# Optimization experiments

Hardware: AMD Instinct MI355X
Metric: run time of the kernel (lower is better)

## Reference

```python
import jax, jax.numpy as jnp
from jax import lax
import numpy as np

B = 2048; D_IN = 784; H = 256; N_OUT = 10

def setup_inputs() -> dict:
    key = jax.random.key(0)
    ks = jax.random.split(key, 12)
    return {
        "x": jax.random.uniform(ks[0], (B, D_IN), jnp.float32),
        "h1": jax.random.randint(ks[1], (B, H), 0, 2, jnp.int32),
        "h2": jax.random.randint(ks[2], (B, H), 0, 2, jnp.int32),
        "y": jax.random.randint(ks[3], (B, N_OUT), 0, 2, jnp.int32),
        "W1": jax.random.normal(ks[4], (D_IN, H), jnp.float32) * 0.05,
        "b1": jnp.zeros((H,), jnp.float32),
        "W2": jax.random.normal(ks[5], (H, H), jnp.float32) * 0.05,
        "b2": jnp.zeros((H,), jnp.float32),
        "Wout": jax.random.normal(ks[6], (H, N_OUT), jnp.float32) * 0.05,
        "bout": jnp.zeros((N_OUT,), jnp.float32),
        # pre-drawn per-node Bernoulli uniforms, shape [H, B] (scan axis first)
        "u1": jax.random.uniform(ks[7], (H, B), jnp.float32),
        "u2": jax.random.uniform(ks[8], (H, B), jnp.float32),
    }

def _sigmoid_ce(labels, logits):
    # tf.nn.sigmoid_cross_entropy_with_logits, numerically stable
    return jnp.maximum(logits, 0.0) - logits * labels + jnp.log1p(jnp.exp(-jnp.abs(logits)))

def _gibbs_layer(pv, cv, nv, W_in, b_in, W_out, b_out, u):
    """One layer of node-by-node Gibbs resampling.
    pv: [B, P] parents, cv: [B, H] current layer (old values),
    nv: [B, Hn] children, u: [H, B] uniforms. Returns (new cv [B,H], final child logits [B,Hn])."""
    parent_logits = pv @ W_in + b_in          # [B, H]; sigmoid(.) = prob_parents
    next_logits0 = cv @ W_out + b_out         # [B, Hn], recurrently updated

    def step(nl, xs):
        node, w_j, pl_j, u_j = xs             # [B], [Hn], [B], [B]
        nl0 = nl - node[:, None] * w_j[None, :]
        nl1 = nl + (1.0 - node)[:, None] * w_j[None, :]
        lp0 = -jnp.sum(_sigmoid_ce(nv, nl0), axis=-1)
        lp1 = -jnp.sum(_sigmoid_ce(nv, nl1), axis=-1)
        # prob = p1/(p1+p0) with p1 = sigm(pl)*exp(lp1), p0 = (1-sigm(pl))*exp(lp0)
        # == sigmoid(pl + lp1 - lp0)  (same math, stable form)
        prob = jax.nn.sigmoid(pl_j + lp1 - lp0)
        new = (u_j < prob).astype(jnp.float32)
        nl_new = jnp.where(new[:, None] > 0.5, nl1, nl0)
        return nl_new, new

    nl_fin, new_T = lax.scan(step, next_logits0, (cv.T, W_out, parent_logits.T, u))
    return new_T.T, nl_fin

def reference(x, h1, h2, y, W1, b1, W2, b2, Wout, bout, u1, u2):
    h1f = h1.astype(jnp.float32)
    h2f = h2.astype(jnp.float32)
    yf = y.astype(jnp.float32)
    # layer 0: parents=x, children=h2 (old values)
    h1_new, _ = _gibbs_layer(x, h1f, h2f, W1, b1, W2, b2, u1)
    # layer 1: parents=h1_new (already updated), children=y, out layer = output_layer
    h2_new, nl_fin = _gibbs_layer(h1_new, h2f, yf, W2, b2, Wout, bout, u2)
    # pack new states + final output-layer logits into one array [B, H+H+N_OUT]
    return jnp.concatenate([h1_new, h2_new, nl_fin], axis=1)
```

## Files before the change

kernel.cpp:

```cpp
#include <hip/hip_runtime.h>
#include <math.h>

#define NB   2048
#define DIN  784
#define HN   256
#define NOUT 10
#define OSTR (HN + HN + NOUT)

struct Smem {
  float4  sup[4][HN];
  double2 tab[65];
  float   scr[4][16 * 20];
  float   h2o[4][HN];
  float   h1n[4][HN];
  float   tmp[4][HN];
  float   yv [4][16];
};

__device__ __forceinline__ float np_expf(float xf) {
  float q = __fmul_rn(xf, 1.442695040888963f);
  q = __fadd_rn(q, 12582912.0f);
  q = __fsub_rn(q, 12582912.0f);
  float x = __builtin_fmaf(q, -6.93145752e-1f, xf);
  x = __builtin_fmaf(q, -1.42860677e-6f, x);
  float num = __builtin_fmaf(x, 5.082762527590693718096e-04f,
                                6.757896990527504603057e-03f);
  num = __builtin_fmaf(num, x, 5.114512081637298353406e-02f);
  num = __builtin_fmaf(num, x, 2.473615434895520810817e-01f);
  num = __builtin_fmaf(num, x, 7.257664613233124478488e-01f);
  num = __builtin_fmaf(num, x, 9.999999999980870924916e-01f);
  float den = __builtin_fmaf(x, 2.159509375685829852307e-02f,
                                -2.742335390411667452936e-01f);
  den = __builtin_fmaf(den, x, 1.0f);
  float r = __fdiv_rn(num, den);
  int qi = (int)q;
  return __fmul_rn(r, __int_as_float((qi + 127) << 23));
}

__device__ __forceinline__ float np_log1pf(float ef, const double2* __restrict__ tab) {
  if (ef < 0x1p-29f) return ef;
  double t  = 1.0 + (double)ef;
  double kd = rint(t * 64.0);
  int   idx = (int)kd - 64;
  double2 te = tab[idx];
  double c  = kd * 0.015625;
  double s  = (t - c) * te.y;
  double p  = fma(s, -1.0/6.0, 0.2);
  p = fma(p, s, -0.25);
  p = fma(p, s,  1.0/3.0);
  p = fma(p, s, -0.5);
  p = fma(p, s,  1.0);
  p = p * s;
  return (float)(te.x + p);
}

__device__ __forceinline__ float ce32(float l, float label, const double2* __restrict__ tab) {
  float t3 = __fsub_rn(fmaxf(l, 0.0f), __fmul_rn(l, label));
  return __fadd_rn(t3, np_log1pf(np_expf(-fabsf(l)), tab));
}

__device__ __forceinline__ bool decide(float u, float ez) {
  float w = __fadd_rn(1.0f, ez);
  float d = __builtin_fmaf(u, w, -1.0f);
  if (__builtin_expect(fabsf(d) < 1e-5f, 0)) {
    float prob = __fdiv_rn(1.0f, w);
    return u < prob;
  }
  return d < 0.0f;
}

template<int CTRL> __device__ __forceinline__ float dppx(float v) {
  return __int_as_float(__builtin_amdgcn_mov_dpp(__float_as_int(v), CTRL, 0xF, 0xF, true));
}
__device__ __forceinline__ float rdl(float v, int l) {
  return __int_as_float(__builtin_amdgcn_readlane(__float_as_int(v), l));
}

__device__ __forceinline__ float sum10(float c) {
  float c0 = rdl(c, 0), c1 = rdl(c, 1), c2 = rdl(c, 2), c3 = rdl(c, 3);
  float c4 = rdl(c, 4), c5 = rdl(c, 5), c6 = rdl(c, 6), c7 = rdl(c, 7);
  float c8 = rdl(c, 8), c9 = rdl(c, 9);
  float t = __fadd_rn(__fadd_rn(__fadd_rn(c0, c1), __fadd_rn(c2, c3)),
                      __fadd_rn(__fadd_rn(c4, c5), __fadd_rn(c6, c7)));
  t = __fadd_rn(t, c8);
  t = __fadd_rn(t, c9);
  return t;
}

__device__ __forceinline__ float fold256_lds(const float c[4], float* __restrict__ scrw,
                                             int idx, int g) {
  *reinterpret_cast<float4*>(scrw + idx * 20 + 4 * g) = make_float4(c[0], c[1], c[2], c[3]);
  const float4* rp = reinterpret_cast<const float4*>(scrw + idx * 20);
  float4 q0 = rp[0], q1 = rp[1], q2 = rp[2], q3 = rp[3];
  float r = q0.x;
  r = __fadd_rn(r, q0.y); r = __fadd_rn(r, q0.z); r = __fadd_rn(r, q0.w);
  r = __fadd_rn(r, q1.x); r = __fadd_rn(r, q1.y); r = __fadd_rn(r, q1.z); r = __fadd_rn(r, q1.w);
  r = __fadd_rn(r, q2.x); r = __fadd_rn(r, q2.y); r = __fadd_rn(r, q2.z); r = __fadd_rn(r, q2.w);
  r = __fadd_rn(r, q3.x); r = __fadd_rn(r, q3.y); r = __fadd_rn(r, q3.z); r = __fadd_rn(r, q3.w);
  r = __fadd_rn(r, dppx<0xB1>(r));
  r = __fadd_rn(r, dppx<0x4E>(r));
  float B0 = rdl(r, 0), B1 = rdl(r, 4), B2 = rdl(r, 8), B3 = rdl(r, 12);
  return __fadd_rn(__fadd_rn(B0, B1), __fadd_rn(B2, B3));
}

__device__ __forceinline__ float fast_sum256(float loc) {
  float r = loc;
  r = r + dppx<0xB1>(r);
  r = r + dppx<0x4E>(r);
  r = r + dppx<0x124>(r);
  r = r + dppx<0x128>(r);
  return (rdl(r, 0) + rdl(r, 16)) + (rdl(r, 32) + rdl(r, 48));
}

__device__ __forceinline__ float lu_of(float u) {
  if (u < 1e-4f || u > 0.9999f) return __int_as_float(0x7FC00000);
  return __logf(u) - __logf(__fsub_rn(1.0f, u));
}

#define ZBAND 0.05f
#define LN2F  0.6931471805599453f

__global__ __launch_bounds__(256) void stoch_mlp(
    const float* __restrict__ x,  const int* __restrict__ h1,
    const int* __restrict__ h2,   const int* __restrict__ y,
    const float* __restrict__ W1, const float* __restrict__ b1,
    const float* __restrict__ W2, const float* __restrict__ b2,
    const float* __restrict__ Wo, const float* __restrict__ bo,
    const float* __restrict__ u1, const float* __restrict__ u2,
    float* __restrict__ out)
{
  __shared__ Smem sm;
  const int t    = threadIdx.x;
  const int lane = t & 63;
  const int wid  = t >> 6;
  const int b0   = blockIdx.x * 4;
  const int b    = b0 + wid;

  if (t < 65) {
    double c = (double)(t + 64) * 0.015625;
    sm.tab[t] = make_double2(log(c), 64.0 / (double)(t + 64));
  }
  for (int j = lane; j < HN; j += 64) sm.h2o[wid][j] = (float)h2[b * HN + j];
  if (lane < 16) sm.yv[wid][lane] = (lane < NOUT) ? (float)y[b * NOUT + lane] : 0.0f;
  {
    float a0 = 0.0f, a1 = 0.0f, a2 = 0.0f, a3 = 0.0f;
    const float* x0 = x + (size_t)b0 * DIN;
    for (int k = 0; k < DIN; ++k) {
      float wk = W1[k * HN + t];
      a0 = __builtin_fmaf(x0[k],           wk, a0);
      a1 = __builtin_fmaf(x0[DIN   + k],   wk, a1);
      a2 = __builtin_fmaf(x0[2*DIN + k],   wk, a2);
      a3 = __builtin_fmaf(x0[3*DIN + k],   wk, a3);
    }
    float bb = b1[t];
    float4 uv = *reinterpret_cast<const float4*>(u1 + (size_t)t * NB + b0);
    float n0 = (float)h1[(b0 + 0) * HN + t];
    float n1 = (float)h1[(b0 + 1) * HN + t];
    float n2 = (float)h1[(b0 + 2) * HN + t];
    float n3 = (float)h1[(b0 + 3) * HN + t];
    sm.sup[0][t] = make_float4(n0, uv.x, __fadd_rn(a0, bb), lu_of(uv.x));
    sm.sup[1][t] = make_float4(n1, uv.y, __fadd_rn(a1, bb), lu_of(uv.y));
    sm.sup[2][t] = make_float4(n2, uv.z, __fadd_rn(a2, bb), lu_of(uv.z));
    sm.sup[3][t] = make_float4(n3, uv.w, __fadd_rn(a3, bb), lu_of(uv.w));
  }
  __syncthreads();

  const double2* tab = sm.tab;
  float* scrw = &sm.scr[wid][0];

  {
    float acc[4] = {0.0f, 0.0f, 0.0f, 0.0f};
    for (int j = 0; j < HN; ++j) {
      float nodej = sm.sup[wid][j].x;
      float4 wf = *reinterpret_cast<const float4*>(W2 + (size_t)j * HN + 4*lane);
      acc[0] = __builtin_fmaf(nodej, wf.x, acc[0]);
      acc[1] = __builtin_fmaf(nodej, wf.y, acc[1]);
      acc[2] = __builtin_fmaf(nodej, wf.z, acc[2]);
      acc[3] = __builtin_fmaf(nodej, wf.w, acc[3]);
    }
    float4 bv = *reinterpret_cast<const float4*>(b2 + 4*lane);
    *reinterpret_cast<float4*>(&sm.tmp[wid][4*lane]) =
        make_float4(__fadd_rn(acc[0], bv.x), __fadd_rn(acc[1], bv.y),
                    __fadd_rn(acc[2], bv.z), __fadd_rn(acc[3], bv.w));
  }

  const int idx  = lane & 15;
  const int g    = lane >> 4;
  const int half = idx >> 3;
  const int jacc = idx & 7;
  const int kb   = half * 128 + (4 * g) * 8 + jacc;

  float nlv[4], nv[4], wv[4];
  int   smk[4];
  #pragma unroll
  for (int i = 0; i < 4; ++i) {
    int k = kb + i * 8;
    nlv[i] = sm.tmp[wid][k];
    nv[i]  = sm.h2o[wid][k];
    smk[i] = (nv[i] != 0.0f) ? (int)0x80000000 : 0;
    wv[i]  = W2[k];
  }
  float S_c;
  {
    float ci[4];
    #pragma unroll
    for (int i = 0; i < 4; ++i) ci[i] = ce32(nlv[i], nv[i], tab);
    S_c = fold256_lds(ci, scrw, idx, g);
  }

  {
    float4 supC = sm.sup[wid][0];
    for (int j = 0; j < HN; ++j) {
      float node = supC.x, uj = supC.y, plj = supC.z, luj = supC.w;
      bool  nd   = (node != 0.0f);
      int   jn   = (j + 1) & (HN - 1);
      float4 supN = sm.sup[wid][jn];
      float wn[4];
      #pragma unroll
      for (int i = 0; i < 4; ++i) wn[i] = W2[(size_t)jn * HN + kb + i * 8];

      int ndm = nd ? (int)0x80000000 : 0;
      float fresh[4], t3[4], p[4];
      #pragma unroll
      for (int i = 0; i < 4; ++i) {
        float ws = __int_as_float(__float_as_int(wv[i]) ^ ndm);
        fresh[i] = __fadd_rn(nlv[i], ws);
        float sl = __int_as_float(__float_as_int(fresh[i]) ^ smk[i]);
        t3[i] = fmaxf(sl, 0.0f);
        p[i]  = __log2f(__fadd_rn(1.0f, __expf(-fabsf(fresh[i]))));
      }
      float T = (t3[0] + t3[1]) + (t3[2] + t3[3]);
      float P = (p[0]  + p[1])  + (p[2]  + p[3]);
      float F = fast_sum256(__builtin_fmaf(LN2F, P, T));
      float sgn = nd ? 1.0f : -1.0f;
      float z = __builtin_fmaf(F - S_c, sgn, plj);
      float d = z - luj;
      bool nw;
      if (__builtin_expect(!(fabsf(d) >= ZBAND), 0)) {
        float one_m = __fsub_rn(1.0f, node);
        float nl0[4], nl1[4], c0i[4], c1i[4];
        #pragma unroll
        for (int i = 0; i < 4; ++i) {
          nl0[i] = __fsub_rn(nlv[i], __fmul_rn(node,  wv[i]));
          nl1[i] = __fadd_rn(nlv[i], __fmul_rn(one_m, wv[i]));
          c0i[i] = ce32(nl0[i], nv[i], tab);
          c1i[i] = ce32(nl1[i], nv[i], tab);
        }
        float S0e = fold256_lds(c0i, scrw, idx, g);
        float S1e = fold256_lds(c1i, scrw, idx, g);
        float ze  = __fsub_rn(__fadd_rn(plj, -S1e), -S0e);
        nw  = decide(uj, np_expf(-ze));
        S_c = nw ? S1e : S0e;
        #pragma unroll
        for (int i = 0; i < 4; ++i) nlv[i] = nw ? nl1[i] : nl0[i];
      } else {
        nw = d > 0.0f;
        bool flip = (nw != nd);
        S_c = flip ? F : S_c;
        #pragma unroll
        for (int i = 0; i < 4; ++i) nlv[i] = flip ? fresh[i] : nlv[i];
      }
      if (lane == 0) sm.h1n[wid][j] = nw ? 1.0f : 0.0f;
      supC = supN;
      #pragma unroll
      for (int i = 0; i < 4; ++i) wv[i] = wn[i];
    }
  }

  {
    float acc[4] = {0.0f, 0.0f, 0.0f, 0.0f};
    for (int j = 0; j < HN; ++j) {
      float nodej = sm.h1n[wid][j];
      float4 wf = *reinterpret_cast<const float4*>(W2 + (size_t)j * HN + 4*lane);
      acc[0] = __builtin_fmaf(nodej, wf.x, acc[0]);
      acc[1] = __builtin_fmaf(nodej, wf.y, acc[1]);
      acc[2] = __builtin_fmaf(nodej, wf.z, acc[2]);
      acc[3] = __builtin_fmaf(nodej, wf.w, acc[3]);
    }
    float4 bv = *reinterpret_cast<const float4*>(b2 + 4*lane);
    float p2[4] = {__fadd_rn(acc[0], bv.x), __fadd_rn(acc[1], bv.y),
                   __fadd_rn(acc[2], bv.z), __fadd_rn(acc[3], bv.w)};
    #pragma unroll
    for (int i = 0; i < 4; ++i) {
      int j = 4 * lane + i;
      float u2v = u2[(size_t)j * NB + b];
      sm.sup[wid][j] = make_float4(sm.h2o[wid][j], u2v, p2[i], lu_of(u2v));
    }
  }

  float nvy = 0.0f, nlo = 0.0f;
  if (lane < NOUT) {
    nvy = sm.yv[wid][lane];
    float a = 0.0f;
    for (int j = 0; j < HN; ++j)
      a = __builtin_fmaf(sm.h2o[wid][j], Wo[j * NOUT + lane], a);
    nlo = __fadd_rn(a, bo[lane]);
  }
  float S_c1 = sum10((lane < NOUT) ? ce32(nlo, nvy, tab) : 0.0f);
  const int  syk  = (nvy != 0.0f) ? (int)0x80000000 : 0;
  const bool lact = (lane < NOUT);

  {
    float w = lact ? Wo[lane] : 0.0f;
    float4 supC = sm.sup[wid][0];
    for (int j = 0; j < HN; ++j) {
      float node = supC.x, uj = supC.y, plj = supC.z, luj = supC.w;
      bool  nd   = (node != 0.0f);
      int   jn   = (j + 1) & (HN - 1);
      float4 supN = sm.sup[wid][jn];
      float wnn = lact ? Wo[jn * NOUT + lane] : 0.0f;
      int ndm = nd ? (int)0x80000000 : 0;
      float ws = __int_as_float(__float_as_int(w) ^ ndm);
      float fresh = __fadd_rn(nlo, ws);
      float sl = __int_as_float(__float_as_int(fresh) ^ syk);
      float t3 = fmaxf(sl, 0.0f);
      float p  = __log2f(__fadd_rn(1.0f, __expf(-fabsf(fresh))));
      float loc = lact ? __builtin_fmaf(LN2F, p, t3) : 0.0f;
      float r = loc;
      r = r + dppx<0xB1>(r);
      r = r + dppx<0x4E>(r);
      float F  = (rdl(r, 0) + rdl(r, 4)) + rdl(r, 8);
      float sgn = nd ? 1.0f : -1.0f;
      float z = __builtin_fmaf(F - S_c1, sgn, plj);
      float d = z - luj;
      bool nw;
      if (__builtin_expect(!(fabsf(d) >= ZBAND), 0)) {
        float one_m = __fsub_rn(1.0f, node);
        float nl0 = __fsub_rn(nlo, __fmul_rn(node,  w));
        float nl1 = __fadd_rn(nlo, __fmul_rn(one_m, w));
        float c0 = lact ? ce32(nl0, nvy, tab) : 0.0f;
        float c1 = lact ? ce32(nl1, nvy, tab) : 0.0f;
        float S0e = sum10(c0);
        float S1e = sum10(c1);
        float ze  = __fsub_rn(__fadd_rn(plj, -S1e), -S0e);
        nw   = decide(uj, np_expf(-ze));
        S_c1 = nw ? S1e : S0e;
        nlo  = nw ? nl1 : nl0;
      } else {
        nw = d > 0.0f;
        bool flip = (nw != nd);
        S_c1 = flip ? F : S_c1;
        nlo  = flip ? fresh : nlo;
      }
      if (lane == 0) out[(size_t)b * OSTR + HN + j] = nw ? 1.0f : 0.0f;
      supC = supN;
      w = wnn;
    }
  }

  float* orow = out + (size_t)b * OSTR;
  for (int j = lane; j < HN; j += 64) orow[j] = sm.h1n[wid][j];
  if (lane < NOUT) orow[2*HN + lane] = nlo;
}

extern "C" void kernel_launch(void* const* d_in, const int* in_sizes, int n_in,
                              void* d_out, int out_size, void* d_ws, size_t ws_size,
                              hipStream_t stream) {
  const float* x  = (const float*)d_in[0];
  const int*   h1 = (const int*)  d_in[1];
  const int*   h2 = (const int*)  d_in[2];
  const int*   y  = (const int*)  d_in[3];
  const float* W1 = (const float*)d_in[4];
  const float* b1 = (const float*)d_in[5];
  const float* W2 = (const float*)d_in[6];
  const float* b2 = (const float*)d_in[7];
  const float* Wo = (const float*)d_in[8];
  const float* bo = (const float*)d_in[9];
  const float* u1 = (const float*)d_in[10];
  const float* u2 = (const float*)d_in[11];
  stoch_mlp<<<NB/4, 256, 0, stream>>>(x, h1, h2, y, W1, b1, W2, b2, Wo, bo, u1, u2,
                                      (float*)d_out);
}
```

Before: 324.5 us.

## Deepen prefetch to two iterations and finish reductions with DPP row ops

Loads of W1, W2, Wo and the per-node LDS records are now software-pipelined two iterations ahead instead of one, and the Gibbs loops are unrolled by two. The aim is to hide global-load latency in the serial node-by-node loops. The 256-lane and 10-lane reductions are finished with extra DPP row-broadcast steps and a single readlane instead of several readlanes and scalar adds. This changes summation order, which could alter the rounding of the logits, and the deeper prefetch uses more registers.

After: 318.6 us (median of 2 runs). No clear change (-1.8%).

```diff
diff --git a/kernel.cpp b/kernel.cpp
--- a/kernel.cpp
+++ b/kernel.cpp
@@ -109,7 +109,9 @@
   r = r + dppx<0x4E>(r);
   r = r + dppx<0x124>(r);
   r = r + dppx<0x128>(r);
-  return (rdl(r, 0) + rdl(r, 16)) + (rdl(r, 32) + rdl(r, 48));
+  r = r + dppx<0x142>(r);
+  r = r + dppx<0x143>(r);
+  return rdl(r, 63);
 }
 
 __device__ __forceinline__ float lu_of(float u) {
@@ -145,12 +147,16 @@
   {
     float a0 = 0.0f, a1 = 0.0f, a2 = 0.0f, a3 = 0.0f;
     const float* x0 = x + (size_t)b0 * DIN;
+    float wk0 = W1[t];
+    float wk1 = W1[HN + t];
     for (int k = 0; k < DIN; ++k) {
-      float wk = W1[k * HN + t];
-      a0 = __builtin_fmaf(x0[k],           wk, a0);
-      a1 = __builtin_fmaf(x0[DIN   + k],   wk, a1);
-      a2 = __builtin_fmaf(x0[2*DIN + k],   wk, a2);
-      a3 = __builtin_fmaf(x0[3*DIN + k],   wk, a3);
+      int k2 = (k + 2 < DIN) ? (k + 2) : 0;
+      float wk2 = W1[(size_t)k2 * HN + t];
+      a0 = __builtin_fmaf(x0[k],           wk0, a0);
+      a1 = __builtin_fmaf(x0[DIN   + k],   wk0, a1);
+      a2 = __builtin_fmaf(x0[2*DIN + k],   wk0, a2);
+      a3 = __builtin_fmaf(x0[3*DIN + k],   wk0, a3);
+      wk0 = wk1; wk1 = wk2;
     }
     float bb = b1[t];
     float4 uv = *reinterpret_cast<const float4*>(u1 + (size_t)t * NB + b0);
@@ -190,7 +196,7 @@
   const int jacc = idx & 7;
   const int kb   = half * 128 + (4 * g) * 8 + jacc;
 
-  float nlv[4], nv[4], wv[4];
+  float nlv[4], nv[4];
   int   smk[4];
   #pragma unroll
   for (int i = 0; i < 4; ++i) {
@@ -198,7 +204,6 @@
     nlv[i] = sm.tmp[wid][k];
     nv[i]  = sm.h2o[wid][k];
     smk[i] = (nv[i] != 0.0f) ? (int)0x80000000 : 0;
-    wv[i]  = W2[k];
   }
   float S_c;
   {
@@ -210,20 +215,28 @@
 
   {
     float4 supC = sm.sup[wid][0];
+    float4 supN = sm.sup[wid][1];
+    float w0[4], w1[4];
+    #pragma unroll
+    for (int i = 0; i < 4; ++i) {
+      w0[i] = W2[kb + i * 8];
+      w1[i] = W2[(size_t)HN + kb + i * 8];
+    }
+    #pragma unroll 2
     for (int j = 0; j < HN; ++j) {
+      int jn2 = (j + 2) & (HN - 1);
+      float4 supN2 = sm.sup[wid][jn2];
+      float wp[4];
+      #pragma unroll
+      for (int i = 0; i < 4; ++i) wp[i] = W2[(size_t)jn2 * HN + kb + i * 8];
+
       float node = supC.x, uj = supC.y, plj = supC.z, luj = supC.w;
       bool  nd   = (node != 0.0f);
-      int   jn   = (j + 1) & (HN - 1);
-      float4 supN = sm.sup[wid][jn];
-      float wn[4];
-      #pragma unroll
-      for (int i = 0; i < 4; ++i) wn[i] = W2[(size_t)jn * HN + kb + i * 8];
-
       int ndm = nd ? (int)0x80000000 : 0;
       float fresh[4], t3[4], p[4];
       #pragma unroll
       for (int i = 0; i < 4; ++i) {
-        float ws = __int_as_float(__float_as_int(wv[i]) ^ ndm);
+        float ws = __int_as_float(__float_as_int(w0[i]) ^ ndm);
         fresh[i] = __fadd_rn(nlv[i], ws);
         float sl = __int_as_float(__float_as_int(fresh[i]) ^ smk[i]);
         t3[i] = fmaxf(sl, 0.0f);
@@ -241,8 +254,8 @@
         float nl0[4], nl1[4], c0i[4], c1i[4];
         #pragma unroll
         for (int i = 0; i < 4; ++i) {
-          nl0[i] = __fsub_rn(nlv[i], __fmul_rn(node,  wv[i]));
-          nl1[i] = __fadd_rn(nlv[i], __fmul_rn(one_m, wv[i]));
+          nl0[i] = __fsub_rn(nlv[i], __fmul_rn(node,  w0[i]));
+          nl1[i] = __fadd_rn(nlv[i], __fmul_rn(one_m, w0[i]));
           c0i[i] = ce32(nl0[i], nv[i], tab);
           c1i[i] = ce32(nl1[i], nv[i], tab);
         }
@@ -261,9 +274,9 @@
         for (int i = 0; i < 4; ++i) nlv[i] = flip ? fresh[i] : nlv[i];
       }
       if (lane == 0) sm.h1n[wid][j] = nw ? 1.0f : 0.0f;
-      supC = supN;
+      supC = supN; supN = supN2;
       #pragma unroll
-      for (int i = 0; i < 4; ++i) wv[i] = wn[i];
+      for (int i = 0; i < 4; ++i) { w0[i] = w1[i]; w1[i] = wp[i]; }
     }
   }
 
@@ -301,16 +314,20 @@
   const bool lact = (lane < NOUT);
 
   {
-    float w = lact ? Wo[lane] : 0.0f;
     float4 supC = sm.sup[wid][0];
+    float4 supN = sm.sup[wid][1];
+    float w0s = lact ? Wo[lane] : 0.0f;
+    float w1s = lact ? Wo[NOUT + lane] : 0.0f;
+    #pragma unroll 2
     for (int j = 0; j < HN; ++j) {
+      int jn2 = (j + 2) & (HN - 1);
+      float4 supN2 = sm.sup[wid][jn2];
+      float wps = lact ? Wo[jn2 * NOUT + lane] : 0.0f;
+
       float node = supC.x, uj = supC.y, plj = supC.z, luj = supC.w;
       bool  nd   = (node != 0.0f);
-      int   jn   = (j + 1) & (HN - 1);
-      float4 supN = sm.sup[wid][jn];
-      float wnn = lact ? Wo[jn * NOUT + lane] : 0.0f;
       int ndm = nd ? (int)0x80000000 : 0;
-      float ws = __int_as_float(__float_as_int(w) ^ ndm);
+      float ws = __int_as_float(__float_as_int(w0s) ^ ndm);
       float fresh = __fadd_rn(nlo, ws);
       float sl = __int_as_float(__float_as_int(fresh) ^ syk);
       float t3 = fmaxf(sl, 0.0f);
@@ -319,15 +336,17 @@
       float r = loc;
       r = r + dppx<0xB1>(r);
       r = r + dppx<0x4E>(r);
-      float F  = (rdl(r, 0) + rdl(r, 4)) + rdl(r, 8);
+      r = r + dppx<0x124>(r);
+      r = r + dppx<0x128>(r);
+      float F  = rdl(r, 0);
       float sgn = nd ? 1.0f : -1.0f;
       float z = __builtin_fmaf(F - S_c1, sgn, plj);
       float d = z - luj;
       bool nw;
       if (__builtin_expect(!(fabsf(d) >= ZBAND), 0)) {
         float one_m = __fsub_rn(1.0f, node);
-        float nl0 = __fsub_rn(nlo, __fmul_rn(node,  w));
-        float nl1 = __fadd_rn(nlo, __fmul_rn(one_m, w));
+        float nl0 = __fsub_rn(nlo, __fmul_rn(node,  w0s));
+        float nl1 = __fadd_rn(nlo, __fmul_rn(one_m, w0s));
         float c0 = lact ? ce32(nl0, nvy, tab) : 0.0f;
         float c1 = lact ? ce32(nl1, nvy, tab) : 0.0f;
         float S0e = sum10(c0);
@@ -343,8 +362,8 @@
         nlo  = flip ? fresh : nlo;
       }
       if (lane == 0) out[(size_t)b * OSTR + HN + j] = nw ? 1.0f : 0.0f;
-      supC = supN;
-      w = wnn;
+      supC = supN; supN = supN2;
+      w0s = w1s; w1s = wps;
     }
   }
 
```
